# Performance work log

Hardware: AMD Instinct MI355X
Metric: run time of the kernel (lower is better)

## Reference

```python
import jax, jax.numpy as jnp
import numpy as np

NUM_HEADS = 8
AGENT_NUM = 64
THETA = 0.7


def conv2d(x, w, pad, groups=1):
    return jax.lax.conv_general_dilated(
        x, w, window_strides=(1, 1), padding=[(pad, pad), (pad, pad)],
        dimension_numbers=("NCHW", "OIHW", "NCHW"), feature_group_count=groups)


def setup_inputs() -> dict:
    key = jax.random.key(0)
    ks = jax.random.split(key, 8)
    B, C, H, W = 8, 256, 64, 64
    return {
        "x": jax.random.normal(ks[0], (B, C, H, W), jnp.float32),
        "qkv_w": jax.random.normal(ks[1], (3 * C, C, 3, 3), jnp.float32) * 0.05,
        "qkv_s": 1.0 + 0.05 * jax.random.normal(ks[2], (3 * C,), jnp.float32),
        "qkv_b": 0.05 * jax.random.normal(ks[3], (3 * C,), jnp.float32),
        "pe_w": jax.random.normal(ks[4], (C, 1, 3, 3), jnp.float32) * 0.05,
        "pe_s": 1.0 + 0.05 * jax.random.normal(ks[5], (C,), jnp.float32),
        "pe_b": 0.05 * jax.random.normal(ks[5], (C,), jnp.float32),
        "proj_w": jax.random.normal(ks[6], (C, C, 1, 1), jnp.float32) * 0.05,
        "proj_s": 1.0 + 0.05 * jax.random.normal(ks[7], (C,), jnp.float32),
        "proj_b": 0.05 * jax.random.normal(ks[7], (C,), jnp.float32),
    }


def reference(x, qkv_w, qkv_s, qkv_b, pe_w, pe_s, pe_b, proj_w, proj_s, proj_b):
    B, C, H, W = x.shape
    h, n = NUM_HEADS, AGENT_NUM
    d = C // h
    scale = d ** -0.5
    ps = int(n ** 0.5)  # pool_size = 8

    # Conv_dif (mode='hv'): normal 3x3 conv minus theta * (1x1 conv with hv-summed weights)
    out_n = conv2d(x, qkv_w, pad=1)
    dif_w = qkv_w.reshape(3 * C, C, 9)[:, :, jnp.array([1, 3, 4, 5, 7])].sum(-1)[:, :, None, None]
    out_d = conv2d(x, dif_w, pad=0)
    qkv = (out_n - THETA * out_d) * qkv_s[:, None, None] + qkv_b[:, None, None]  # folded BN

    q, k, v = jnp.split(qkv, 3, axis=1)  # each [B, C, H, W]
    qh = q.reshape(B, h, d, H * W)
    kh = k.reshape(B, h, d, H * W)
    vh = v.reshape(B, h, d, H * W)

    # adaptive avg pool q -> agent tokens (exact block mean since H,W % ps == 0)
    a = q.reshape(B, C, ps, H // ps, ps, W // ps).mean(axis=(3, 5))  # [B, C, ps, ps]
    a = a.reshape(B, C, n).transpose(0, 2, 1).reshape(B, n, h, d).transpose(0, 2, 3, 1)  # [B,h,d,n]

    # stage 1: agents attend to keys, aggregate values
    attn_k = jax.nn.softmax(jnp.einsum("bhdn,bhdN->bhnN", a, kh) * scale, axis=-1)
    attn = jnp.einsum("bhnN,bhdN->bhnd", attn_k, vh)  # [B,h,n,d]

    # stage 2: queries attend to agents
    q_attn = jax.nn.softmax(jnp.einsum("bhdN,bhdn->bhNn", qh, a) * scale, axis=-1)
    out = jnp.einsum("bhNn,bhnd->bhdN", q_attn, attn).reshape(B, C, H, W)

    # depthwise positional encoding on v (BN folded)
    pe = conv2d(v, pe_w, pad=1, groups=C) * pe_s[:, None, None] + pe_b[:, None, None]
    out = out + pe

    # 1x1 projection (BN folded, Identity act)
    out = conv2d(out, proj_w, pad=0) * proj_s[:, None, None] + proj_b[:, None, None]
    return out
```

## Files before the change

### kernel.cpp

```cpp
#include <hip/hip_runtime.h>
#include <cstdint>

typedef __attribute__((ext_vector_type(8))) short short8;
typedef __attribute__((ext_vector_type(4))) float f32x4;

#define THETA 0.7f
#define SCALE 0.17677669529663687f

__device__ __forceinline__ ushort f2b(float f) {
    uint32_t u = __float_as_uint(f);
    u += 0x7FFFu + ((u >> 16) & 1u);
    return (ushort)(u >> 16);
}
__device__ __forceinline__ float b2f(ushort b) {
    return __uint_as_float(((uint32_t)b) << 16);
}

__global__ __launch_bounds__(256) void k_pad(const float* __restrict__ x, ushort* __restrict__ xp) {
    int b = blockIdx.x >> 6, y = blockIdx.x & 63;
    int t = threadIdx.x;
    __shared__ float buf[64][65];
    for (int cc = 0; cc < 4; ++cc) {
        __syncthreads();
#pragma unroll
        for (int i = 0; i < 16; ++i) {
            int idx = i * 256 + t;
            int c = idx >> 6, xx = idx & 63;
            buf[c][xx] = x[(((size_t)b * 256 + cc * 64 + c) << 12) + (y << 6) + xx];
        }
        __syncthreads();
#pragma unroll
        for (int i = 0; i < 16; ++i) {
            int idx = i * 256 + t;
            int xx = idx >> 6, c = idx & 63;
            xp[((size_t)(b * 66 + y + 1) * 66 + (xx + 1)) * 256 + cc * 64 + c] = f2b(buf[c][xx]);
        }
    }
}

__global__ __launch_bounds__(256) void k_foldw(const float* __restrict__ w, const float* __restrict__ s,
                                               ushort* __restrict__ Wa) {
    int o = blockIdx.x, c = threadIdx.x;
    const float* wp = w + ((size_t)o * 256 + c) * 9;
    float v[9];
#pragma unroll
    for (int p = 0; p < 9; ++p) v[p] = wp[p];
    float hv = v[1] + v[3] + v[4] + v[5] + v[7];
    v[4] -= THETA * hv;
    float sc = s[o];
#pragma unroll
    for (int p = 0; p < 9; ++p)
        Wa[(size_t)o * 2304 + p * 256 + c] = f2b(v[p] * sc);
}

__global__ __launch_bounds__(256) void k_foldp(const float* __restrict__ w, const float* __restrict__ s,
                                               ushort* __restrict__ Wh, ushort* __restrict__ Wl) {
    int o = blockIdx.x, c = threadIdx.x;
    float v = w[(size_t)o * 256 + c] * s[o];
    ushort hi = f2b(v);
    Wh[(size_t)o * 256 + c] = hi;
    Wl[(size_t)o * 256 + c] = f2b(v - b2f(hi));
}

__global__ __launch_bounds__(256) void k_conv(const ushort* __restrict__ xp, const ushort* __restrict__ Wa,
                                              const float* __restrict__ qbias, ushort* __restrict__ qkv) {
    __shared__ ushort Al[128][40];
    __shared__ ushort Bl[128][40];
    const int t = threadIdx.x;
    const int bid0 = blockIdx.x;
    const int bid = (bid0 & 7) * 192 + (bid0 >> 3);
    const int b = bid / 192;
    const int ob = (bid % 192) >> 5;
    const int pb = bid & 31;
    const int o0 = ob << 7;
    const int lane = t & 63;
    const int w = t >> 6;
    const int rw = t >> 2;
    const int q4 = t & 3;
    const ushort* Ag0 = Wa + (size_t)(o0 + rw) * 2304 + q4 * 8;
    const ushort* Ag1 = Ag0 + (size_t)64 * 2304;
    const int y0 = pb * 2;
    const size_t xb = (size_t)b * 66 * 66 * 256;

    f32x4 acc[4][4] = {};

    const int ow2 = (w >> 1) << 6;
    const int pw2 = (w & 1) << 6;
    const int fr = lane & 15;
    const int fs = (lane >> 4) << 3;

    uint4 ra0, ra1, rb0, rb1;
    auto loadk = [&](int kn) {
        int pp = kn >> 3;
        int c0 = (kn & 7) << 5;
        int ky = pp / 3, kx = pp - ky * 3;
        ra0 = *(const uint4*)(Ag0 + kn * 32);
        ra1 = *(const uint4*)(Ag1 + kn * 32);
        const ushort* bp = xp + xb + ((size_t)((y0 + ky) * 66 + (rw + kx))) * 256 + c0 + q4 * 8;
        rb0 = *(const uint4*)bp;
        rb1 = *(const uint4*)(bp + 66 * 256);
    };
    loadk(0);
    for (int kc = 0; kc < 72; ++kc) {
        if (kc) __syncthreads();
        *(uint4*)&Al[rw][q4 * 8] = ra0;
        *(uint4*)&Al[rw + 64][q4 * 8] = ra1;
        *(uint4*)&Bl[rw][q4 * 8] = rb0;
        *(uint4*)&Bl[rw + 64][q4 * 8] = rb1;
        __syncthreads();
        if (kc < 71) loadk(kc + 1);
        short8 af[4], bf[4];
#pragma unroll
        for (int i = 0; i < 4; ++i) af[i] = *(const short8*)&Al[ow2 + i * 16 + fr][fs];
#pragma unroll
        for (int j = 0; j < 4; ++j) bf[j] = *(const short8*)&Bl[pw2 + j * 16 + fr][fs];
#pragma unroll
        for (int i = 0; i < 4; ++i)
#pragma unroll
            for (int j = 0; j < 4; ++j)
                acc[i][j] = __builtin_amdgcn_mfma_f32_16x16x32_bf16(af[i], bf[j], acc[i][j], 0, 0, 0);
    }
    const int pbase = pb * 128 + pw2 + (lane & 15);
#pragma unroll
    for (int i = 0; i < 4; ++i) {
        int o = o0 + ow2 + i * 16 + (lane >> 4) * 4;
#pragma unroll
        for (int r = 0; r < 4; ++r) {
            float bias = qbias[o + r];
            ushort* dst = qkv + ((size_t)b * 768 + o + r) * 4096 + pbase;
#pragma unroll
            for (int j = 0; j < 4; ++j)
                dst[j * 16] = f2b(acc[i][j][r] + bias);
        }
    }
}

__global__ __launch_bounds__(256) void k_pool(const ushort* __restrict__ qkv, float* __restrict__ ap) {
    const int bid = blockIdx.x;
    const int b = bid >> 8, c = bid & 255;
    const int t = threadIdx.x;
    const int y = t >> 2, xq = t & 3;
    __shared__ float lp[64][8];
    const ushort* qp = qkv + ((size_t)b * 768 + c) * 4096 + y * 64 + xq * 16;
    short8 a0 = *(const short8*)(qp);
    short8 a1 = *(const short8*)(qp + 8);
    float s0 = 0, s1 = 0;
#pragma unroll
    for (int j = 0; j < 8; ++j) s0 += b2f((ushort)a0[j]);
#pragma unroll
    for (int j = 0; j < 8; ++j) s1 += b2f((ushort)a1[j]);
    lp[y][xq * 2] = s0;
    lp[y][xq * 2 + 1] = s1;
    __syncthreads();
    if (t < 64) {
        int py = t >> 3, px = t & 7;
        float s = 0;
#pragma unroll
        for (int r = 0; r < 8; ++r) s += lp[py * 8 + r][px];
        ap[((size_t)b * 256 + c) * 64 + t] = s * (1.0f / 64.0f);
    }
}

__global__ __launch_bounds__(256, 2) void k_att1(const ushort* __restrict__ qkv, const float* __restrict__ ap,
                                                 float* __restrict__ attn_g, float* __restrict__ s_g) {
    const int bid0 = blockIdx.x;
    const int bid = (bid0 & 7) * 128 + (bid0 >> 3);
    const int seg = bid & 15, h = (bid >> 4) & 7, b = bid >> 7;
    const int t = threadIdx.x;
    const int lane = t & 63, w = t >> 6;
    const int fr = lane & 15, fs = (lane >> 4) << 3;
    const int g4 = (lane >> 4) << 2;
    const int pixseg = seg << 8;

    __shared__ ushort a_lds[64][40];
    __shared__ ushort kt[256][40];
    __shared__ ushort pt[64][264];

#pragma unroll
    for (int i = 0; i < 8; ++i) {
        int e = i * 256 + t;
        int n = e & 63, d = e >> 6;
        a_lds[n][d] = f2b(ap[((size_t)b * 256 + h * 32 + d) * 64 + n] * SCALE);
    }
    const ushort* kb = qkv + ((size_t)b * 768 + 256 + h * 32) * 4096;
    const ushort* vb = qkv + ((size_t)b * 768 + 512 + h * 32) * 4096;
#pragma unroll
    for (int i = 0; i < 4; ++i) {
        int e = i * 256 + t;
        int d = e & 31, oc = e >> 5;
        const ushort* src = kb + (size_t)d * 4096 + pixseg + oc * 8;
        short8 v = *(const short8*)src;
#pragma unroll
        for (int j2 = 0; j2 < 8; ++j2) kt[oc * 8 + j2][d] = (ushort)v[j2];
    }
    __syncthreads();

    f32x4 accL[4][4];
    {
        short8 af[4], bq[4];
#pragma unroll
        for (int i = 0; i < 4; ++i) af[i] = *(const short8*)&a_lds[i * 16 + fr][fs];
#pragma unroll
        for (int j = 0; j < 4; ++j) bq[j] = *(const short8*)&kt[w * 64 + j * 16 + fr][fs];
#pragma unroll
        for (int i = 0; i < 4; ++i)
#pragma unroll
            for (int j = 0; j < 4; ++j) {
                f32x4 z = {0.f, 0.f, 0.f, 0.f};
                accL[i][j] = __builtin_amdgcn_mfma_f32_16x16x32_bf16(af[i], bq[j], z, 0, 0, 0);
            }
    }
    float sreg[4][4];
#pragma unroll
    for (int i = 0; i < 4; ++i)
#pragma unroll
        for (int r = 0; r < 4; ++r) sreg[i][r] = 0.f;
#pragma unroll
    for (int i = 0; i < 4; ++i)
#pragma unroll
        for (int j = 0; j < 4; ++j) {
            int pixl = w * 64 + j * 16 + fr;
#pragma unroll
            for (int r = 0; r < 4; ++r) {
                float e = __expf(accL[i][j][r]);
                sreg[i][r] += e;
                pt[i * 16 + g4 + r][pixl] = f2b(e);
            }
        }
#pragma unroll
    for (int i = 0; i < 4; ++i)
#pragma unroll
        for (int r = 0; r < 4; ++r) {
            float s = sreg[i][r];
            s += __shfl_xor(s, 1);
            s += __shfl_xor(s, 2);
            s += __shfl_xor(s, 4);
            s += __shfl_xor(s, 8);
            sreg[i][r] = s;
        }
    if (fr == 0) {
#pragma unroll
        for (int i = 0; i < 4; ++i)
#pragma unroll
            for (int r = 0; r < 4; ++r)
                atomicAdd(&s_g[((size_t)b * 8 + h) * 64 + i * 16 + g4 + r], sreg[i][r]);
    }
    __syncthreads();

    f32x4 accO[4][2] = {};
#pragma unroll
    for (int ks = 0; ks < 2; ++ks) {
        int pixk = w * 64 + ks * 32 + fs;
        short8 af[4], bf[2];
#pragma unroll
        for (int i = 0; i < 4; ++i) af[i] = *(const short8*)&pt[i * 16 + fr][pixk];
#pragma unroll
        for (int dt = 0; dt < 2; ++dt)
            bf[dt] = *(const short8*)(vb + (size_t)(dt * 16 + fr) * 4096 + pixseg + pixk);
#pragma unroll
        for (int i = 0; i < 4; ++i)
#pragma unroll
            for (int dt = 0; dt < 2; ++dt)
                accO[i][dt] = __builtin_amdgcn_mfma_f32_16x16x32_bf16(af[i], bf[dt], accO[i][dt], 0, 0, 0);
    }
#pragma unroll
    for (int i = 0; i < 4; ++i)
#pragma unroll
        for (int dt = 0; dt < 2; ++dt)
#pragma unroll
            for (int r = 0; r < 4; ++r) {
                int n = i * 16 + g4 + r;
                int d = dt * 16 + fr;
                atomicAdd(&attn_g[(((size_t)b * 8 + h) * 64 + n) * 32 + d], accO[i][dt][r]);
            }
}

__global__ __launch_bounds__(256, 2) void k_att2(const ushort* __restrict__ qkv, const float* __restrict__ ap,
                                                 const float* __restrict__ attn_g, const float* __restrict__ s_g,
                                                 ushort* __restrict__ outp) {
    const int bid0 = blockIdx.x;
    const int bid = (bid0 & 7) * 256 + (bid0 >> 3);
    const int ch = bid & 31, h = (bid >> 5) & 7, b = bid >> 8;
    const int t = threadIdx.x;
    const int lane = t & 63, w = t >> 6;
    const int fr = lane & 15, fs = (lane >> 4) << 3;
    const int pw = w << 5;
    const int pix0 = ch << 7;

    __shared__ ushort a_lds[64][40];
    __shared__ ushort qt[128][40];
    __shared__ ushort pt[128][72];
    __shared__ ushort gh[32][72];
    __shared__ ushort gl[32][72];
    __shared__ float sInv[64];

#pragma unroll
    for (int i = 0; i < 8; ++i) {
        int e = i * 256 + t;
        int n = e & 63, d = e >> 6;
        a_lds[n][d] = f2b(ap[((size_t)b * 256 + h * 32 + d) * 64 + n] * SCALE);
    }
    if (t < 64) sInv[t] = 1.0f / s_g[((size_t)b * 8 + h) * 64 + t];
#pragma unroll
    for (int i = 0; i < 2; ++i) {
        int e = i * 256 + t;
        int d = e & 31, oc = e >> 5;
        const ushort* src = qkv + ((size_t)b * 768 + h * 32 + d) * 4096 + pix0 + oc * 8;
        short8 v = *(const short8*)src;
#pragma unroll
        for (int j2 = 0; j2 < 8; ++j2) qt[oc * 8 + j2][d] = (ushort)v[j2];
    }
    __syncthreads();

#pragma unroll
    for (int i = 0; i < 8; ++i) {
        int e = i * 256 + t;
        int n = e >> 5, d = e & 31;
        float g = attn_g[(((size_t)b * 8 + h) * 64 + n) * 32 + d] * sInv[n];
        ushort hi = f2b(g);
        gh[d][n] = hi;
        gl[d][n] = f2b(g - b2f(hi));
    }

    f32x4 accL[4][2];
    {
        short8 af[4], bq[2];
#pragma unroll
        for (int i = 0; i < 4; ++i) af[i] = *(const short8*)&a_lds[i * 16 + fr][fs];
#pragma unroll
        for (int j = 0; j < 2; ++j) bq[j] = *(const short8*)&qt[pw + j * 16 + fr][fs];
#pragma unroll
        for (int i = 0; i < 4; ++i)
#pragma unroll
            for (int j = 0; j < 2; ++j) {
                f32x4 z = {0.f, 0.f, 0.f, 0.f};
                accL[i][j] = __builtin_amdgcn_mfma_f32_16x16x32_bf16(af[i], bq[j], z, 0, 0, 0);
            }
    }
    float sj[2];
#pragma unroll
    for (int j = 0; j < 2; ++j) {
        float s = 0.f;
        int pix = pw + j * 16 + fr;
#pragma unroll
        for (int i = 0; i < 4; ++i) {
            float e0 = __expf(accL[i][j][0]);
            float e1 = __expf(accL[i][j][1]);
            float e2 = __expf(accL[i][j][2]);
            float e3 = __expf(accL[i][j][3]);
            s += (e0 + e1) + (e2 + e3);
            int n0 = i * 16 + (lane >> 4) * 4;
            *(uint32_t*)&pt[pix][n0] = (uint32_t)f2b(e0) | ((uint32_t)f2b(e1) << 16);
            *(uint32_t*)&pt[pix][n0 + 2] = (uint32_t)f2b(e2) | ((uint32_t)f2b(e3) << 16);
        }
        s += __shfl_xor(s, 16);
        s += __shfl_xor(s, 32);
        sj[j] = 1.0f / s;
    }
    __syncthreads();

    f32x4 accO[2][2] = {};
#pragma unroll
    for (int ks = 0; ks < 2; ++ks) {
        short8 gah[2], gal[2], pa[2];
#pragma unroll
        for (int dt = 0; dt < 2; ++dt) {
            gah[dt] = *(const short8*)&gh[dt * 16 + fr][ks * 32 + fs];
            gal[dt] = *(const short8*)&gl[dt * 16 + fr][ks * 32 + fs];
        }
#pragma unroll
        for (int j = 0; j < 2; ++j) pa[j] = *(const short8*)&pt[pw + j * 16 + fr][ks * 32 + fs];
#pragma unroll
        for (int dt = 0; dt < 2; ++dt)
#pragma unroll
            for (int j = 0; j < 2; ++j) {
                accO[dt][j] = __builtin_amdgcn_mfma_f32_16x16x32_bf16(gah[dt], pa[j], accO[dt][j], 0, 0, 0);
                accO[dt][j] = __builtin_amdgcn_mfma_f32_16x16x32_bf16(gal[dt], pa[j], accO[dt][j], 0, 0, 0);
            }
    }
#pragma unroll
    for (int dt = 0; dt < 2; ++dt)
#pragma unroll
        for (int j = 0; j < 2; ++j) {
            int pix = pix0 + pw + j * 16 + fr;
#pragma unroll
            for (int r = 0; r < 4; ++r) {
                int d = dt * 16 + (lane >> 4) * 4 + r;
                outp[((size_t)b * 256 + h * 32 + d) * 4096 + pix] = f2b(accO[dt][j][r] * sj[j]);
            }
        }
}

__global__ __launch_bounds__(256) void k_pe(const ushort* __restrict__ qkv, const float* __restrict__ pw,
                                            const float* __restrict__ ps, const float* __restrict__ pbias,
                                            ushort* __restrict__ outp) {
    int gid = blockIdx.x * 256 + threadIdx.x;
    int x4 = (gid & 15) << 2;
    int y = (gid >> 4) & 63;
    int c = (gid >> 10) & 255;
    int b = gid >> 18;
    const ushort* vp = qkv + ((size_t)b * 768 + 512 + c) * 4096;
    const float* wp = pw + c * 9;
    float s0 = 0, s1 = 0, s2 = 0, s3 = 0;
#pragma unroll
    for (int ky = 0; ky < 3; ++ky) {
        int yy = y + ky - 1;
        if ((unsigned)yy >= 64u) continue;
        const ushort* rp = vp + yy * 64 + x4;
        ushort4 m = *(const ushort4*)rp;
        float m0 = b2f(m.x), m1 = b2f(m.y), m2 = b2f(m.z), m3 = b2f(m.w);
        float lft = (x4 > 0) ? b2f(rp[-1]) : 0.f;
        float rgt = (x4 < 60) ? b2f(rp[4]) : 0.f;
        float w0 = wp[ky * 3], w1 = wp[ky * 3 + 1], w2 = wp[ky * 3 + 2];
        s0 += w0 * lft + w1 * m0 + w2 * m1;
        s1 += w0 * m0 + w1 * m1 + w2 * m2;
        s2 += w0 * m1 + w1 * m2 + w2 * m3;
        s3 += w0 * m2 + w1 * m3 + w2 * rgt;
    }
    float sc = ps[c], bb = pbias[c];
    ushort* op = outp + ((size_t)b * 256 + c) * 4096 + y * 64 + x4;
    ushort4 o = *(ushort4*)op;
    o.x = f2b(b2f(o.x) + sc * s0 + bb);
    o.y = f2b(b2f(o.y) + sc * s1 + bb);
    o.z = f2b(b2f(o.z) + sc * s2 + bb);
    o.w = f2b(b2f(o.w) + sc * s3 + bb);
    *(ushort4*)op = o;
}

__global__ __launch_bounds__(256) void k_proj(const ushort* __restrict__ outp, const ushort* __restrict__ Wh,
                                              const ushort* __restrict__ Wl, const float* __restrict__ pbias,
                                              float* __restrict__ out) {
    __shared__ ushort Ah[128][40];
    __shared__ ushort Alo[128][40];
    __shared__ ushort Xl[32][132];
    const int t = threadIdx.x;
    const int bid0 = blockIdx.x;
    const int bid = (bid0 & 7) * 64 + (bid0 >> 3);
    const int b = bid >> 6;
    const int ob = (bid >> 5) & 1;
    const int pb = bid & 31;
    const int o0 = ob << 7;
    const int p0 = pb << 7;
    const int lane = t & 63;
    const int w = t >> 6;
    const int rw = t >> 2, q4 = t & 3;
    const int cl = t >> 3, pg = t & 7;
    const int ow2 = (w >> 1) << 6;
    const int pw2 = (w & 1) << 6;
    const int fr = lane & 15;
    const int fs = (lane >> 4) << 3;

    f32x4 acc[4][4] = {};
    uint4 rah0, rah1, ral0, ral1, rx0, rx1;
    auto loadk = [&](int kc) {
        const size_t awoff = (size_t)(o0 + rw) * 256 + kc * 32 + q4 * 8;
        rah0 = *(const uint4*)(Wh + awoff);
        rah1 = *(const uint4*)(Wh + awoff + (size_t)64 * 256);
        ral0 = *(const uint4*)(Wl + awoff);
        ral1 = *(const uint4*)(Wl + awoff + (size_t)64 * 256);
        const ushort* xsrc = outp + ((size_t)b * 256 + kc * 32 + cl) * 4096 + p0 + pg * 16;
        rx0 = *(const uint4*)xsrc;
        rx1 = *(const uint4*)(xsrc + 8);
    };
    loadk(0);
    for (int kc = 0; kc < 8; ++kc) {
        if (kc) __syncthreads();
        *(uint4*)&Ah[rw][q4 * 8] = rah0;
        *(uint4*)&Ah[rw + 64][q4 * 8] = rah1;
        *(uint4*)&Alo[rw][q4 * 8] = ral0;
        *(uint4*)&Alo[rw + 64][q4 * 8] = ral1;
        *(uint4*)&Xl[cl][pg * 16] = rx0;
        *(uint4*)&Xl[cl][pg * 16 + 8] = rx1;
        __syncthreads();
        if (kc < 7) loadk(kc + 1);
        short8 ah[4], al[4], bf[4];
#pragma unroll
        for (int i = 0; i < 4; ++i) {
            ah[i] = *(const short8*)&Ah[ow2 + i * 16 + fr][fs];
            al[i] = *(const short8*)&Alo[ow2 + i * 16 + fr][fs];
        }
#pragma unroll
        for (int j = 0; j < 4; ++j) {
            int pl = pw2 + j * 16 + fr;
#pragma unroll
            for (int kk = 0; kk < 8; ++kk) bf[j][kk] = (short)Xl[fs + kk][pl];
        }
#pragma unroll
        for (int i = 0; i < 4; ++i)
#pragma unroll
            for (int j = 0; j < 4; ++j) {
                acc[i][j] = __builtin_amdgcn_mfma_f32_16x16x32_bf16(ah[i], bf[j], acc[i][j], 0, 0, 0);
                acc[i][j] = __builtin_amdgcn_mfma_f32_16x16x32_bf16(al[i], bf[j], acc[i][j], 0, 0, 0);
            }
    }
    const int pbase = p0 + pw2 + (lane & 15);
#pragma unroll
    for (int i = 0; i < 4; ++i) {
        int o = o0 + ow2 + i * 16 + (lane >> 4) * 4;
#pragma unroll
        for (int r = 0; r < 4; ++r) {
            float bias = pbias[o + r];
            float* dst = out + ((size_t)b * 256 + o + r) * 4096 + pbase;
#pragma unroll
            for (int j = 0; j < 4; ++j)
                dst[j * 16] = acc[i][j][r] + bias;
        }
    }
}

extern "C" void kernel_launch(void* const* d_in, const int* in_sizes, int n_in,
                              void* d_out, int out_size, void* d_ws, size_t ws_size,
                              hipStream_t stream) {
    const float* x = (const float*)d_in[0];
    const float* qkv_w = (const float*)d_in[1];
    const float* qkv_s = (const float*)d_in[2];
    const float* qkv_b = (const float*)d_in[3];
    const float* pe_w = (const float*)d_in[4];
    const float* pe_s = (const float*)d_in[5];
    const float* pe_b = (const float*)d_in[6];
    const float* proj_w = (const float*)d_in[7];
    const float* proj_s = (const float*)d_in[8];
    const float* proj_b = (const float*)d_in[9];
    float* out = (float*)d_out;

    char* ws = (char*)d_ws;
    ushort* xp = (ushort*)(ws);
    ushort* Wa = (ushort*)(ws + 17842176);
    ushort* qkvb = (ushort*)(ws + 21381120);
    float* apool = (float*)(ws + 71712768);
    float* attn_g = (float*)(ws + 72237056);
    float* s_g = (float*)(ws + 72761344);
    ushort* outpb = (ushort*)(ws + 72777728);
    ushort* Wh = (ushort*)(ws + 89554944);
    ushort* Wl = (ushort*)(ws + 89686016);

    hipMemsetAsync(xp, 0, 17842176, stream);
    hipMemsetAsync(attn_g, 0, 524288 + 16384, stream);
    k_pad<<<512, 256, 0, stream>>>(x, xp);
    k_foldw<<<768, 256, 0, stream>>>(qkv_w, qkv_s, Wa);
    k_foldp<<<256, 256, 0, stream>>>(proj_w, proj_s, Wh, Wl);
    k_conv<<<1536, 256, 0, stream>>>(xp, Wa, qkv_b, qkvb);
    k_pool<<<2048, 256, 0, stream>>>(qkvb, apool);
    k_att1<<<1024, 256, 0, stream>>>(qkvb, apool, attn_g, s_g);
    k_att2<<<2048, 256, 0, stream>>>(qkvb, apool, attn_g, s_g, outpb);
    k_pe<<<8192, 256, 0, stream>>>(qkvb, pe_w, pe_s, pe_b, outpb);
    k_proj<<<512, 256, 0, stream>>>(outpb, Wh, Wl, proj_b, out);
}
```

Measured before the change: 390.1 us.

## Fuse depthwise PE into att2, store channel-last output, and drop LDS staging in proj

Folds the depthwise 3x3 positional-encoding conv into the stage-2 attention kernel by staging a halo of V rows in shared memory, which removes the separate k_pe launch and its read-modify-write of the output. The attention output is now written in pixel-major, channel-contiguous layout, so the projection GEMM loads its MFMA operands straight from global memory without shared-memory staging or barriers. Also vectorizes the pad kernel's bf16 stores and coalesces the weight-fold loads through shared memory. The cost is more shared memory and extra per-element PE arithmetic in att2, which could reduce occupancy, and the proj kernel loses software prefetching.

```diff
diff --git a/kernel.cpp b/kernel.cpp
--- a/kernel.cpp
+++ b/kernel.cpp
@@ -30,27 +30,35 @@
         }
         __syncthreads();
 #pragma unroll
-        for (int i = 0; i < 16; ++i) {
-            int idx = i * 256 + t;
-            int xx = idx >> 6, c = idx & 63;
-            xp[((size_t)(b * 66 + y + 1) * 66 + (xx + 1)) * 256 + cc * 64 + c] = f2b(buf[c][xx]);
+        for (int i = 0; i < 4; ++i) {
+            int idx = i * 1024 + t * 4;
+            int xx = idx >> 6, c0 = idx & 63;
+            ushort4 u;
+            u.x = f2b(buf[c0][xx]);
+            u.y = f2b(buf[c0 + 1][xx]);
+            u.z = f2b(buf[c0 + 2][xx]);
+            u.w = f2b(buf[c0 + 3][xx]);
+            *(ushort4*)&xp[((size_t)(b * 66 + y + 1) * 66 + (xx + 1)) * 256 + cc * 64 + c0] = u;
         }
     }
 }
 
 __global__ __launch_bounds__(256) void k_foldw(const float* __restrict__ w, const float* __restrict__ s,
                                                ushort* __restrict__ Wa) {
-    int o = blockIdx.x, c = threadIdx.x;
-    const float* wp = w + ((size_t)o * 256 + c) * 9;
+    int o = blockIdx.x, t = threadIdx.x;
+    __shared__ float lw[2304];
+#pragma unroll
+    for (int i = 0; i < 9; ++i) lw[i * 256 + t] = w[(size_t)o * 2304 + i * 256 + t];
+    __syncthreads();
     float v[9];
 #pragma unroll
-    for (int p = 0; p < 9; ++p) v[p] = wp[p];
+    for (int p = 0; p < 9; ++p) v[p] = lw[t * 9 + p];
     float hv = v[1] + v[3] + v[4] + v[5] + v[7];
     v[4] -= THETA * hv;
     float sc = s[o];
 #pragma unroll
     for (int p = 0; p < 9; ++p)
-        Wa[(size_t)o * 2304 + p * 256 + c] = f2b(v[p] * sc);
+        Wa[(size_t)o * 2304 + p * 256 + t] = f2b(v[p] * sc);
 }
 
 __global__ __launch_bounds__(256) void k_foldp(const float* __restrict__ w, const float* __restrict__ s,
@@ -277,13 +285,15 @@
 
 __global__ __launch_bounds__(256, 2) void k_att2(const ushort* __restrict__ qkv, const float* __restrict__ ap,
                                                  const float* __restrict__ attn_g, const float* __restrict__ s_g,
-                                                 ushort* __restrict__ outp) {
+                                                 const float* __restrict__ pe_w, const float* __restrict__ pe_s,
+                                                 const float* __restrict__ pe_b, ushort* __restrict__ outp) {
     const int bid0 = blockIdx.x;
     const int bid = (bid0 & 7) * 256 + (bid0 >> 3);
     const int ch = bid & 31, h = (bid >> 5) & 7, b = bid >> 8;
     const int t = threadIdx.x;
     const int lane = t & 63, w = t >> 6;
     const int fr = lane & 15, fs = (lane >> 4) << 3;
+    const int g4 = (lane >> 4) << 2;
     const int pw = w << 5;
     const int pix0 = ch << 7;
 
@@ -292,6 +302,9 @@
     __shared__ ushort pt[128][72];
     __shared__ ushort gh[32][72];
     __shared__ ushort gl[32][72];
+    __shared__ ushort vsh[32][264];
+    __shared__ float wsh[32][9];
+    __shared__ float psh[32], pbsh[32];
     __shared__ float sInv[64];
 
 #pragma unroll
@@ -301,6 +314,26 @@
         a_lds[n][d] = f2b(ap[((size_t)b * 256 + h * 32 + d) * 64 + n] * SCALE);
     }
     if (t < 64) sInv[t] = 1.0f / s_g[((size_t)b * 8 + h) * 64 + t];
+    if (t < 32) {
+        int c = h * 32 + t;
+#pragma unroll
+        for (int p = 0; p < 9; ++p) wsh[t][p] = pe_w[c * 9 + p];
+        psh[t] = pe_s[c];
+        pbsh[t] = pe_b[c];
+    }
+    {
+        int d = t >> 3, part = t & 7;
+        const ushort* vsrc = qkv + ((size_t)b * 768 + 512 + h * 32 + d) * 4096;
+        int yh = (pix0 >> 6) - 1;
+        uint4 zz;
+        zz.x = zz.y = zz.z = zz.w = 0u;
+#pragma unroll
+        for (int m = 0; m < 4; ++m) {
+            int row = yh + m;
+            uint4 val = (row >= 0 && row <= 63) ? *(const uint4*)(vsrc + row * 64 + part * 8) : zz;
+            *(uint4*)&vsh[d][m * 64 + part * 8] = val;
+        }
+    }
 #pragma unroll
     for (int i = 0; i < 2; ++i) {
         int e = i * 256 + t;
@@ -349,7 +382,7 @@
             float e2 = __expf(accL[i][j][2]);
             float e3 = __expf(accL[i][j][3]);
             s += (e0 + e1) + (e2 + e3);
-            int n0 = i * 16 + (lane >> 4) * 4;
+            int n0 = i * 16 + g4;
             *(uint32_t*)&pt[pix][n0] = (uint32_t)f2b(e0) | ((uint32_t)f2b(e1) << 16);
             *(uint32_t*)&pt[pix][n0 + 2] = (uint32_t)f2b(e2) | ((uint32_t)f2b(e3) << 16);
         }
@@ -382,57 +415,37 @@
     for (int dt = 0; dt < 2; ++dt)
 #pragma unroll
         for (int j = 0; j < 2; ++j) {
-            int pix = pix0 + pw + j * 16 + fr;
+            int pixl = pw + j * 16 + fr;
+            int pix = pix0 + pixl;
+            int x = pix & 63;
+            int lr = (pixl >> 6) + 1;
+            ushort4 o4;
+            float vals[4];
 #pragma unroll
             for (int r = 0; r < 4; ++r) {
-                int d = dt * 16 + (lane >> 4) * 4 + r;
-                outp[((size_t)b * 256 + h * 32 + d) * 4096 + pix] = f2b(accO[dt][j][r] * sj[j]);
-            }
-        }
-}
-
-__global__ __launch_bounds__(256) void k_pe(const ushort* __restrict__ qkv, const float* __restrict__ pw,
-                                            const float* __restrict__ ps, const float* __restrict__ pbias,
-                                            ushort* __restrict__ outp) {
-    int gid = blockIdx.x * 256 + threadIdx.x;
-    int x4 = (gid & 15) << 2;
-    int y = (gid >> 4) & 63;
-    int c = (gid >> 10) & 255;
-    int b = gid >> 18;
-    const ushort* vp = qkv + ((size_t)b * 768 + 512 + c) * 4096;
-    const float* wp = pw + c * 9;
-    float s0 = 0, s1 = 0, s2 = 0, s3 = 0;
-#pragma unroll
-    for (int ky = 0; ky < 3; ++ky) {
-        int yy = y + ky - 1;
-        if ((unsigned)yy >= 64u) continue;
-        const ushort* rp = vp + yy * 64 + x4;
-        ushort4 m = *(const ushort4*)rp;
-        float m0 = b2f(m.x), m1 = b2f(m.y), m2 = b2f(m.z), m3 = b2f(m.w);
-        float lft = (x4 > 0) ? b2f(rp[-1]) : 0.f;
-        float rgt = (x4 < 60) ? b2f(rp[4]) : 0.f;
-        float w0 = wp[ky * 3], w1 = wp[ky * 3 + 1], w2 = wp[ky * 3 + 2];
-        s0 += w0 * lft + w1 * m0 + w2 * m1;
-        s1 += w0 * m0 + w1 * m1 + w2 * m2;
-        s2 += w0 * m1 + w1 * m2 + w2 * m3;
-        s3 += w0 * m2 + w1 * m3 + w2 * rgt;
-    }
-    float sc = ps[c], bb = pbias[c];
-    ushort* op = outp + ((size_t)b * 256 + c) * 4096 + y * 64 + x4;
-    ushort4 o = *(ushort4*)op;
-    o.x = f2b(b2f(o.x) + sc * s0 + bb);
-    o.y = f2b(b2f(o.y) + sc * s1 + bb);
-    o.z = f2b(b2f(o.z) + sc * s2 + bb);
-    o.w = f2b(b2f(o.w) + sc * s3 + bb);
-    *(ushort4*)op = o;
-}
-
-__global__ __launch_bounds__(256) void k_proj(const ushort* __restrict__ outp, const ushort* __restrict__ Wh,
+                int d = dt * 16 + g4 + r;
+                float pe = 0.f;
+#pragma unroll
+                for (int ky = 0; ky < 3; ++ky) {
+                    int base = (lr - 1 + ky) * 64 + x;
+                    float M = b2f(vsh[d][base]);
+                    float L = (x > 0) ? b2f(vsh[d][base - 1]) : 0.f;
+                    float R = (x < 63) ? b2f(vsh[d][base + 1]) : 0.f;
+                    pe += wsh[d][ky * 3] * L + wsh[d][ky * 3 + 1] * M + wsh[d][ky * 3 + 2] * R;
+                }
+                vals[r] = accO[dt][j][r] * sj[j] + psh[d] * pe + pbsh[d];
+            }
+            o4.x = f2b(vals[0]);
+            o4.y = f2b(vals[1]);
+            o4.z = f2b(vals[2]);
+            o4.w = f2b(vals[3]);
+            *(ushort4*)&outp[((size_t)(b << 12) + pix) * 256 + h * 32 + dt * 16 + g4] = o4;
+        }
+}
+
+__global__ __launch_bounds__(256) void k_proj(const ushort* __restrict__ xT, const ushort* __restrict__ Wh,
                                               const ushort* __restrict__ Wl, const float* __restrict__ pbias,
                                               float* __restrict__ out) {
-    __shared__ ushort Ah[128][40];
-    __shared__ ushort Alo[128][40];
-    __shared__ ushort Xl[32][132];
     const int t = threadIdx.x;
     const int bid0 = blockIdx.x;
     const int bid = (bid0 & 7) * 64 + (bid0 >> 3);
@@ -443,48 +456,27 @@
     const int p0 = pb << 7;
     const int lane = t & 63;
     const int w = t >> 6;
-    const int rw = t >> 2, q4 = t & 3;
-    const int cl = t >> 3, pg = t & 7;
     const int ow2 = (w >> 1) << 6;
     const int pw2 = (w & 1) << 6;
     const int fr = lane & 15;
     const int fs = (lane >> 4) << 3;
 
+    const ushort* Ap = Wh + (size_t)(o0 + ow2 + fr) * 256 + fs;
+    const ushort* Lp = Wl + (size_t)(o0 + ow2 + fr) * 256 + fs;
+    const ushort* Bp = xT + ((size_t)(b << 12) + p0 + pw2 + fr) * 256 + fs;
+
     f32x4 acc[4][4] = {};
-    uint4 rah0, rah1, ral0, ral1, rx0, rx1;
-    auto loadk = [&](int kc) {
-        const size_t awoff = (size_t)(o0 + rw) * 256 + kc * 32 + q4 * 8;
-        rah0 = *(const uint4*)(Wh + awoff);
-        rah1 = *(const uint4*)(Wh + awoff + (size_t)64 * 256);
-        ral0 = *(const uint4*)(Wl + awoff);
-        ral1 = *(const uint4*)(Wl + awoff + (size_t)64 * 256);
-        const ushort* xsrc = outp + ((size_t)b * 256 + kc * 32 + cl) * 4096 + p0 + pg * 16;
-        rx0 = *(const uint4*)xsrc;
-        rx1 = *(const uint4*)(xsrc + 8);
-    };
-    loadk(0);
+#pragma unroll 2
     for (int kc = 0; kc < 8; ++kc) {
-        if (kc) __syncthreads();
-        *(uint4*)&Ah[rw][q4 * 8] = rah0;
-        *(uint4*)&Ah[rw + 64][q4 * 8] = rah1;
-        *(uint4*)&Alo[rw][q4 * 8] = ral0;
-        *(uint4*)&Alo[rw + 64][q4 * 8] = ral1;
-        *(uint4*)&Xl[cl][pg * 16] = rx0;
-        *(uint4*)&Xl[cl][pg * 16 + 8] = rx1;
-        __syncthreads();
-        if (kc < 7) loadk(kc + 1);
         short8 ah[4], al[4], bf[4];
 #pragma unroll
         for (int i = 0; i < 4; ++i) {
-            ah[i] = *(const short8*)&Ah[ow2 + i * 16 + fr][fs];
-            al[i] = *(const short8*)&Alo[ow2 + i * 16 + fr][fs];
-        }
-#pragma unroll
-        for (int j = 0; j < 4; ++j) {
-            int pl = pw2 + j * 16 + fr;
-#pragma unroll
-            for (int kk = 0; kk < 8; ++kk) bf[j][kk] = (short)Xl[fs + kk][pl];
-        }
+            ah[i] = *(const short8*)(Ap + (size_t)(i * 16) * 256 + kc * 32);
+            al[i] = *(const short8*)(Lp + (size_t)(i * 16) * 256 + kc * 32);
+        }
+#pragma unroll
+        for (int j = 0; j < 4; ++j)
+            bf[j] = *(const short8*)(Bp + (size_t)(j * 16) * 256 + kc * 32);
 #pragma unroll
         for (int i = 0; i < 4; ++i)
 #pragma unroll
@@ -493,7 +485,7 @@
                 acc[i][j] = __builtin_amdgcn_mfma_f32_16x16x32_bf16(al[i], bf[j], acc[i][j], 0, 0, 0);
             }
     }
-    const int pbase = p0 + pw2 + (lane & 15);
+    const int pbase = p0 + pw2 + fr;
 #pragma unroll
     for (int i = 0; i < 4; ++i) {
         int o = o0 + ow2 + i * 16 + (lane >> 4) * 4;
@@ -530,7 +522,7 @@
     float* apool = (float*)(ws + 71712768);
     float* attn_g = (float*)(ws + 72237056);
     float* s_g = (float*)(ws + 72761344);
-    ushort* outpb = (ushort*)(ws + 72777728);
+    ushort* outp_t = (ushort*)(ws + 72777728);
     ushort* Wh = (ushort*)(ws + 89554944);
     ushort* Wl = (ushort*)(ws + 89686016);
 
@@ -542,7 +534,6 @@
     k_conv<<<1536, 256, 0, stream>>>(xp, Wa, qkv_b, qkvb);
     k_pool<<<2048, 256, 0, stream>>>(qkvb, apool);
     k_att1<<<1024, 256, 0, stream>>>(qkvb, apool, attn_g, s_g);
-    k_att2<<<2048, 256, 0, stream>>>(qkvb, apool, attn_g, s_g, outpb);
-    k_pe<<<8192, 256, 0, stream>>>(qkvb, pe_w, pe_s, pe_b, outpb);
-    k_proj<<<512, 256, 0, stream>>>(outpb, Wh, Wl, proj_b, out);
-}
+    k_att2<<<2048, 256, 0, stream>>>(qkvb, apool, attn_g, s_g, pe_w, pe_s, pe_b, outp_t);
+    k_proj<<<512, 256, 0, stream>>>(outp_t, Wh, Wl, proj_b, out);
+}
```

Result: no change. 396.8 us (+1.7%).
